# Performance work log

Measured on AMD Instinct MI355X. Metric: run time of the kernel, lower is better.

Reference implementation:

```python
import jax, jax.numpy as jnp
import numpy as np

T, S, F, A, POS = 32, 4096, 256, 64, 128


def setup_inputs() -> dict:
    key = jax.random.key(0)
    ks = jax.random.split(key, 12)
    sc = lambda fan_in: 1.0 / np.sqrt(fan_in)
    return {
        "batch_data": jax.random.normal(ks[0], (T * S, F), dtype=jnp.float32),
        "xywh": jax.random.uniform(ks[1], (T * S, 4), dtype=jnp.float32),
        # nn.Linear params (y = x @ W.T + b)
        "Wa": jax.random.uniform(ks[2], (A, F), minval=-sc(F), maxval=sc(F)),
        "ba": jax.random.uniform(ks[3], (A,), minval=-sc(F), maxval=sc(F)),
        "Wb": jax.random.uniform(ks[4], (A, F), minval=-sc(F), maxval=sc(F)),
        "bb": jax.random.uniform(ks[5], (A,), minval=-sc(F), maxval=sc(F)),
        "Wg": jax.random.uniform(ks[6], (F, F), minval=-sc(F), maxval=sc(F)),
        "bg": jax.random.uniform(ks[7], (F,), minval=-sc(F), maxval=sc(F)),
        "Wh": jax.random.uniform(ks[8], (POS, 2), minval=-sc(2), maxval=sc(2)),
        "bh": jax.random.uniform(ks[9], (POS,), minval=-sc(2), maxval=sc(2)),
    }


def reference(batch_data, xywh, Wa, ba, Wb, bb, Wg, bg, Wh, bh):
    x = batch_data.reshape(T, S, F)
    pos = xywh.reshape(T, S, -1)
    # positional embedding path (computed in original forward but unused in output)
    avg_pos = jnp.mean(pos, axis=0)            # [S, 4]
    rel_pos = pos[:, :, :2] - avg_pos[:, :2]   # [T, S, 2]
    _pos_embeds = rel_pos @ Wh.T + bh          # [T, S, POS] (dead, matches source)

    theta = x @ Wa.T + ba                      # [T, S, A]
    phi = x @ Wb.T + bb                        # [T, S, A]
    feats = x @ Wg.T + bg                      # [T, S, F]

    # per-object temporal attention: attn[s, t, u] = theta[t, s] . phi[u, s]
    attn = jnp.einsum('tsa,usa->stu', theta, phi)       # [S, T, T]
    out = jnp.einsum('stu,usf->tsf', attn, feats)       # [T, S, F]
    return out
```

## Files before the change

kernel.cpp:

```cpp
#include <hip/hip_runtime.h>

#define T_ 32
#define S_ 4096
#define F_ 256
#define A_ 64

typedef __attribute__((ext_vector_type(8))) short s8v;
typedef __attribute__((ext_vector_type(4))) float f4v;
typedef __attribute__((ext_vector_type(4))) short s4v;

#define MFMA(a, b, c) __builtin_amdgcn_mfma_f32_16x16x32_bf16((a), (b), (c), 0, 0, 0)

__device__ __forceinline__ unsigned short f2bf(float f) {
    unsigned int u = __builtin_bit_cast(unsigned int, f);
    u += 0x7FFFu + ((u >> 16) & 1u);
    return (unsigned short)(u >> 16);
}

__global__ void convert_weights(const float* __restrict__ Wa,
                                const float* __restrict__ Wb,
                                const float* __restrict__ Wg,
                                unsigned short* __restrict__ wsB)
{
    int base = (blockIdx.x * 256 + threadIdx.x) * 4;
    const float* src;
    if (base < 16384)      src = Wa + base;
    else if (base < 32768) src = Wb + (base - 16384);
    else                   src = Wg + (base - 32768);
    float4 v = *(const float4*)src;
    s4v p;
    p[0] = (short)f2bf(v.x); p[1] = (short)f2bf(v.y);
    p[2] = (short)f2bf(v.z); p[3] = (short)f2bf(v.w);
    *(s4v*)(wsB + base) = p;
}

#define XS_OFF 0
#define TH_OFF 16384
#define PH_OFF 20480
#define AT_OFF 24576
#define FT_OFF 26624
#define LDS_BYTES 43008

__global__ __launch_bounds__(256, 4) void fused_temporal(
    const float* __restrict__ X,
    const unsigned short* __restrict__ wsB,
    const float* __restrict__ ba, const float* __restrict__ bb,
    const float* __restrict__ bg,
    float* __restrict__ out)
{
    __shared__ alignas(16) unsigned char smem[LDS_BYTES];
    const int tid  = threadIdx.x;
    const int wave = tid >> 6;
    const int lane = tid & 63;
    const int quad = lane >> 4;
    const int l15  = lane & 15;
    const int s    = blockIdx.x;

    const unsigned short* WaB = wsB;
    const unsigned short* WbB = wsB + 16384;
    const unsigned short* WgB = wsB + 32768;

    float4 xv[8];
    #pragma unroll
    for (int i = 0; i < 4; ++i) {
        int linear = i * 256 + tid;
        int t = linear >> 5;
        int c = linear & 31;
        const float* xp = X + ((size_t)(t * S_ + s)) * F_ + c * 8;
        xv[2 * i]     = *(const float4*)(xp);
        xv[2 * i + 1] = *(const float4*)(xp + 4);
    }

    s8v wafrag[8], wbfrag[8];
    {
        const unsigned short* wa_row = WaB + (size_t)(16 * wave + l15) * F_ + quad * 8;
        const unsigned short* wb_row = WbB + (size_t)(16 * wave + l15) * F_ + quad * 8;
        #pragma unroll
        for (int ks = 0; ks < 8; ++ks) {
            wafrag[ks] = *(const s8v*)(wa_row + ks * 32);
            wbfrag[ks] = *(const s8v*)(wb_row + ks * 32);
        }
    }

    #pragma unroll
    for (int i = 0; i < 4; ++i) {
        int linear = i * 256 + tid;
        int t = linear >> 5;
        int c = linear & 31;
        float4 v0 = xv[2 * i];
        float4 v1 = xv[2 * i + 1];
        s8v p;
        p[0] = (short)f2bf(v0.x); p[1] = (short)f2bf(v0.y);
        p[2] = (short)f2bf(v0.z); p[3] = (short)f2bf(v0.w);
        p[4] = (short)f2bf(v1.x); p[5] = (short)f2bf(v1.y);
        p[6] = (short)f2bf(v1.z); p[7] = (short)f2bf(v1.w);
        *(s8v*)(&smem[XS_OFF + t * 512 + (((c + t) & 31) << 4)]) = p;
    }
    __syncthreads();

    s8v wg[2][8];
    {
        f4v ta0 = {0.f,0.f,0.f,0.f}, ta1 = {0.f,0.f,0.f,0.f};
        f4v pa0 = {0.f,0.f,0.f,0.f}, pa1 = {0.f,0.f,0.f,0.f};
        #pragma unroll
        for (int ks = 0; ks < 8; ++ks) {
            int chunk = 4 * ks + quad;
            s8v a0 = *(const s8v*)(&smem[XS_OFF + l15 * 512 + (((chunk + l15) & 31) << 4)]);
            s8v a1 = *(const s8v*)(&smem[XS_OFF + (l15 + 16) * 512 + (((chunk + l15 + 16) & 31) << 4)]);
            ta0 = MFMA(a0, wafrag[ks], ta0);
            ta1 = MFMA(a1, wafrag[ks], ta1);
            pa0 = MFMA(a0, wbfrag[ks], pa0);
            pa1 = MFMA(a1, wbfrag[ks], pa1);
        }

        #pragma unroll
        for (int g = 0; g < 2; ++g) {
            const unsigned short* wg_row = WgB + (size_t)(64 * wave + 16 * g + l15) * F_ + quad * 8;
            #pragma unroll
            for (int ks = 0; ks < 8; ++ks) wg[g][ks] = *(const s8v*)(wg_row + ks * 32);
        }

        float biasa = ba[16 * wave + l15];
        float biasb = bb[16 * wave + l15];
        int a_col = 16 * wave + l15;
        int chunk = a_col >> 3;
        int sub   = (a_col & 7) * 2;
        #pragma unroll
        for (int mt = 0; mt < 2; ++mt) {
            f4v va = mt ? ta1 : ta0;
            f4v vb = mt ? pa1 : pa0;
            #pragma unroll
            for (int r = 0; r < 4; ++r) {
                int t  = quad * 4 + r + 16 * mt;
                int sw = ((chunk + t) & 7) << 4;
                *(unsigned short*)(&smem[TH_OFF + t * 128 + sw + sub]) = f2bf(va[r] + biasa);
                *(unsigned short*)(&smem[PH_OFF + t * 128 + sw + sub]) = f2bf(vb[r] + biasb);
            }
        }
    }
    __syncthreads();

    {
        int mt2 = wave >> 1, nt2 = wave & 1;
        int t2 = l15 + 16 * mt2;
        int u2 = l15 + 16 * nt2;
        f4v acc2 = {0.f,0.f,0.f,0.f};
        #pragma unroll
        for (int ks = 0; ks < 2; ++ks) {
            int chunk = 4 * ks + quad;
            s8v av = *(const s8v*)(&smem[TH_OFF + t2 * 128 + (((chunk + t2) & 7) << 4)]);
            s8v bv = *(const s8v*)(&smem[PH_OFF + u2 * 128 + (((chunk + u2) & 7) << 4)]);
            acc2 = MFMA(av, bv, acc2);
        }
        int chunk = u2 >> 3;
        int sub   = (u2 & 7) * 2;
        #pragma unroll
        for (int r = 0; r < 4; ++r) {
            int tt = quad * 4 + r + 16 * mt2;
            *(unsigned short*)(&smem[AT_OFF + tt * 64 + (((chunk + tt) & 3) << 4) + sub]) = f2bf(acc2[r]);
        }
    }
    __syncthreads();

    {
        s8v battn[2];
        #pragma unroll
        for (int nt = 0; nt < 2; ++nt) {
            int t = l15 + 16 * nt;
            battn[nt] = *(const s8v*)(&smem[AT_OFF + t * 64 + (((quad + t) & 3) << 4)]);
        }

        #pragma unroll
        for (int g = 0; g < 4; ++g) {
            int n0 = 64 * wave + 16 * g;
            f4v fa0 = {0.f,0.f,0.f,0.f}, fa1 = {0.f,0.f,0.f,0.f};
            #pragma unroll
            for (int ks = 0; ks < 8; ++ks) {
                int chunk = 4 * ks + quad;
                s8v a0 = *(const s8v*)(&smem[XS_OFF + l15 * 512 + (((chunk + l15) & 31) << 4)]);
                s8v a1 = *(const s8v*)(&smem[XS_OFF + (l15 + 16) * 512 + (((chunk + l15 + 16) & 31) << 4)]);
                fa0 = MFMA(a0, wg[g & 1][ks], fa0);
                fa1 = MFMA(a1, wg[g & 1][ks], fa1);
            }
            if (g < 2) {
                const unsigned short* wg_row = WgB + (size_t)(64 * wave + 16 * (g + 2) + l15) * F_ + quad * 8;
                #pragma unroll
                for (int ks = 0; ks < 8; ++ks) wg[g & 1][ks] = *(const s8v*)(wg_row + ks * 32);
            }

            float biasg = bg[n0 + l15];
            int f = n0 + l15;
            #pragma unroll
            for (int mt = 0; mt < 2; ++mt) {
                f4v v = mt ? fa1 : fa0;
                int u0 = quad * 4 + 16 * mt;
                s4v pk;
                #pragma unroll
                for (int r = 0; r < 4; ++r) pk[r] = (short)f2bf(v[r] + biasg);
                int addr = FT_OFF + f * 64 + ((((u0 >> 3) + f) & 3) << 4) + (u0 & 7) * 2;
                *(s4v*)(&smem[addr]) = pk;
            }

            s8v av = *(const s8v*)(&smem[FT_OFF + f * 64 + (((quad + f) & 3) << 4)]);
            int f0 = n0 + 4 * quad;
            #pragma unroll
            for (int nt = 0; nt < 2; ++nt) {
                f4v z = {0.f,0.f,0.f,0.f};
                f4v acc = MFMA(av, battn[nt], z);
                int t = l15 + 16 * nt;
                float4 st;
                st.x = acc[0]; st.y = acc[1]; st.z = acc[2]; st.w = acc[3];
                *(float4*)(out + ((size_t)(t * S_ + s)) * F_ + f0) = st;
            }
        }
    }
}

extern "C" void kernel_launch(void* const* d_in, const int* in_sizes, int n_in,
                              void* d_out, int out_size, void* d_ws, size_t ws_size,
                              hipStream_t stream) {
    (void)in_sizes; (void)n_in; (void)ws_size; (void)out_size;
    const float* X  = (const float*)d_in[0];
    const float* Wa = (const float*)d_in[2];
    const float* ba = (const float*)d_in[3];
    const float* Wb = (const float*)d_in[4];
    const float* bb = (const float*)d_in[5];
    const float* Wg = (const float*)d_in[6];
    const float* bg = (const float*)d_in[7];
    float* out = (float*)d_out;
    unsigned short* wsB = (unsigned short*)d_ws;

    convert_weights<<<dim3(96), dim3(256), 0, stream>>>(Wa, Wb, Wg, wsB);
    fused_temporal<<<dim3(S_), dim3(256), 0, stream>>>(X, wsB, ba, bb, bg, out);
}
```

Before: 322.2 us.

## Process two objects per block to amortize weight fragment loads

Each block now handles two spatial positions (64 rows) instead of one, so every Wa/Wb/Wg fragment loaded from global memory feeds twice as many MFMAs. The LDS layout is reorganized so the feats staging area reuses the theta/phi region and is private to each wave. The grid is halved and launch bounds drop from 4 to 3 blocks per CU because of the larger LDS footprint and register use. The X prefetch is no longer overlapped with the weight loads, which may expose more memory latency.

```diff
diff --git a/kernel.cpp b/kernel.cpp
--- a/kernel.cpp
+++ b/kernel.cpp
@@ -4,6 +4,7 @@
 #define S_ 4096
 #define F_ 256
 #define A_ 64
+#define NS 2
 
 typedef __attribute__((ext_vector_type(8))) short s8v;
 typedef __attribute__((ext_vector_type(4))) float f4v;
@@ -35,13 +36,13 @@
 }
 
 #define XS_OFF 0
-#define TH_OFF 16384
-#define PH_OFF 20480
-#define AT_OFF 24576
-#define FT_OFF 26624
-#define LDS_BYTES 43008
-
-__global__ __launch_bounds__(256, 4) void fused_temporal(
+#define TH_OFF 32768
+#define PH_OFF 40960
+#define AT_OFF 49152
+#define FT_OFF 32768
+#define LDS_BYTES 53248
+
+__global__ __launch_bounds__(256, 3) void fused_temporal(
     const float* __restrict__ X,
     const unsigned short* __restrict__ wsB,
     const float* __restrict__ ba, const float* __restrict__ bb,
@@ -54,63 +55,59 @@
     const int lane = tid & 63;
     const int quad = lane >> 4;
     const int l15  = lane & 15;
-    const int s    = blockIdx.x;
+    const int s0   = blockIdx.x * NS;
 
     const unsigned short* WaB = wsB;
     const unsigned short* WbB = wsB + 16384;
     const unsigned short* WgB = wsB + 32768;
 
-    float4 xv[8];
     #pragma unroll
-    for (int i = 0; i < 4; ++i) {
+    for (int i = 0; i < 8; ++i) {
         int linear = i * 256 + tid;
-        int t = linear >> 5;
+        int r = linear >> 5;
         int c = linear & 31;
-        const float* xp = X + ((size_t)(t * S_ + s)) * F_ + c * 8;
-        xv[2 * i]     = *(const float4*)(xp);
-        xv[2 * i + 1] = *(const float4*)(xp + 4);
-    }
-
-    s8v wafrag[8], wbfrag[8];
-    {
-        const unsigned short* wa_row = WaB + (size_t)(16 * wave + l15) * F_ + quad * 8;
-        const unsigned short* wb_row = WbB + (size_t)(16 * wave + l15) * F_ + quad * 8;
-        #pragma unroll
-        for (int ks = 0; ks < 8; ++ks) {
-            wafrag[ks] = *(const s8v*)(wa_row + ks * 32);
-            wbfrag[ks] = *(const s8v*)(wb_row + ks * 32);
-        }
-    }
-
-    #pragma unroll
-    for (int i = 0; i < 4; ++i) {
-        int linear = i * 256 + tid;
-        int t = linear >> 5;
-        int c = linear & 31;
-        float4 v0 = xv[2 * i];
-        float4 v1 = xv[2 * i + 1];
+        int t  = r & 31;
+        int sl = r >> 5;
+        const float* xp = X + ((size_t)(t * S_ + s0 + sl)) * F_ + c * 8;
+        float4 v0 = *(const float4*)(xp);
+        float4 v1 = *(const float4*)(xp + 4);
         s8v p;
         p[0] = (short)f2bf(v0.x); p[1] = (short)f2bf(v0.y);
         p[2] = (short)f2bf(v0.z); p[3] = (short)f2bf(v0.w);
         p[4] = (short)f2bf(v1.x); p[5] = (short)f2bf(v1.y);
         p[6] = (short)f2bf(v1.z); p[7] = (short)f2bf(v1.w);
-        *(s8v*)(&smem[XS_OFF + t * 512 + (((c + t) & 31) << 4)]) = p;
+        *(s8v*)(&smem[XS_OFF + r * 512 + (((c + r) & 31) << 4)]) = p;
     }
     __syncthreads();
 
     s8v wg[2][8];
     {
-        f4v ta0 = {0.f,0.f,0.f,0.f}, ta1 = {0.f,0.f,0.f,0.f};
-        f4v pa0 = {0.f,0.f,0.f,0.f}, pa1 = {0.f,0.f,0.f,0.f};
+        const int n0 = 16 * wave;
+        s8v wafrag[8], wbfrag[8];
+        {
+            const unsigned short* wa_row = WaB + (size_t)(n0 + l15) * F_ + quad * 8;
+            const unsigned short* wb_row = WbB + (size_t)(n0 + l15) * F_ + quad * 8;
+            #pragma unroll
+            for (int ks = 0; ks < 8; ++ks) {
+                wafrag[ks] = *(const s8v*)(wa_row + ks * 32);
+                wbfrag[ks] = *(const s8v*)(wb_row + ks * 32);
+            }
+        }
+
+        f4v ta[4], pa[4];
+        #pragma unroll
+        for (int mt = 0; mt < 4; ++mt) { ta[mt] = f4v{0.f,0.f,0.f,0.f}; pa[mt] = f4v{0.f,0.f,0.f,0.f}; }
+
         #pragma unroll
         for (int ks = 0; ks < 8; ++ks) {
             int chunk = 4 * ks + quad;
-            s8v a0 = *(const s8v*)(&smem[XS_OFF + l15 * 512 + (((chunk + l15) & 31) << 4)]);
-            s8v a1 = *(const s8v*)(&smem[XS_OFF + (l15 + 16) * 512 + (((chunk + l15 + 16) & 31) << 4)]);
-            ta0 = MFMA(a0, wafrag[ks], ta0);
-            ta1 = MFMA(a1, wafrag[ks], ta1);
-            pa0 = MFMA(a0, wbfrag[ks], pa0);
-            pa1 = MFMA(a1, wbfrag[ks], pa1);
+            #pragma unroll
+            for (int mt = 0; mt < 4; ++mt) {
+                int r = 16 * mt + l15;
+                s8v a = *(const s8v*)(&smem[XS_OFF + r * 512 + (((chunk + r) & 31) << 4)]);
+                ta[mt] = MFMA(a, wafrag[ks], ta[mt]);
+                pa[mt] = MFMA(a, wbfrag[ks], pa[mt]);
+            }
         }
 
         #pragma unroll
@@ -120,67 +117,81 @@
             for (int ks = 0; ks < 8; ++ks) wg[g][ks] = *(const s8v*)(wg_row + ks * 32);
         }
 
-        float biasa = ba[16 * wave + l15];
-        float biasb = bb[16 * wave + l15];
-        int a_col = 16 * wave + l15;
+        float biasa = ba[n0 + l15];
+        float biasb = bb[n0 + l15];
+        int a_col = n0 + l15;
         int chunk = a_col >> 3;
         int sub   = (a_col & 7) * 2;
         #pragma unroll
-        for (int mt = 0; mt < 2; ++mt) {
-            f4v va = mt ? ta1 : ta0;
-            f4v vb = mt ? pa1 : pa0;
+        for (int mt = 0; mt < 4; ++mt) {
             #pragma unroll
             for (int r = 0; r < 4; ++r) {
-                int t  = quad * 4 + r + 16 * mt;
-                int sw = ((chunk + t) & 7) << 4;
-                *(unsigned short*)(&smem[TH_OFF + t * 128 + sw + sub]) = f2bf(va[r] + biasa);
-                *(unsigned short*)(&smem[PH_OFF + t * 128 + sw + sub]) = f2bf(vb[r] + biasb);
+                int row = 16 * mt + quad * 4 + r;
+                int sw  = ((chunk + row) & 7) << 4;
+                *(unsigned short*)(&smem[TH_OFF + row * 128 + sw + sub]) = f2bf(ta[mt][r] + biasa);
+                *(unsigned short*)(&smem[PH_OFF + row * 128 + sw + sub]) = f2bf(pa[mt][r] + biasb);
             }
         }
     }
     __syncthreads();
 
     {
-        int mt2 = wave >> 1, nt2 = wave & 1;
-        int t2 = l15 + 16 * mt2;
-        int u2 = l15 + 16 * nt2;
-        f4v acc2 = {0.f,0.f,0.f,0.f};
-        #pragma unroll
-        for (int ks = 0; ks < 2; ++ks) {
-            int chunk = 4 * ks + quad;
-            s8v av = *(const s8v*)(&smem[TH_OFF + t2 * 128 + (((chunk + t2) & 7) << 4)]);
-            s8v bv = *(const s8v*)(&smem[PH_OFF + u2 * 128 + (((chunk + u2) & 7) << 4)]);
-            acc2 = MFMA(av, bv, acc2);
-        }
-        int chunk = u2 >> 3;
-        int sub   = (u2 & 7) * 2;
-        #pragma unroll
-        for (int r = 0; r < 4; ++r) {
-            int tt = quad * 4 + r + 16 * mt2;
-            *(unsigned short*)(&smem[AT_OFF + tt * 64 + (((chunk + tt) & 3) << 4) + sub]) = f2bf(acc2[r]);
+        int sl  = wave >> 1;
+        int mt2 = wave & 1;
+        int t2  = l15 + 16 * mt2;
+        int rth = sl * 32 + t2;
+        #pragma unroll
+        for (int nt2 = 0; nt2 < 2; ++nt2) {
+            int u2  = l15 + 16 * nt2;
+            int rph = sl * 32 + u2;
+            f4v acc2 = {0.f,0.f,0.f,0.f};
+            #pragma unroll
+            for (int ks = 0; ks < 2; ++ks) {
+                int chunk = 4 * ks + quad;
+                s8v av = *(const s8v*)(&smem[TH_OFF + rth * 128 + (((chunk + rth) & 7) << 4)]);
+                s8v bv = *(const s8v*)(&smem[PH_OFF + rph * 128 + (((chunk + rph) & 7) << 4)]);
+                acc2 = MFMA(av, bv, acc2);
+            }
+            int chunk = u2 >> 3;
+            int sub   = (u2 & 7) * 2;
+            #pragma unroll
+            for (int r = 0; r < 4; ++r) {
+                int tt  = quad * 4 + r + 16 * mt2;
+                int rat = sl * 32 + tt;
+                *(unsigned short*)(&smem[AT_OFF + rat * 64 + (((chunk + rat) & 3) << 4) + sub]) = f2bf(acc2[r]);
+            }
         }
     }
     __syncthreads();
 
     {
-        s8v battn[2];
-        #pragma unroll
-        for (int nt = 0; nt < 2; ++nt) {
-            int t = l15 + 16 * nt;
-            battn[nt] = *(const s8v*)(&smem[AT_OFF + t * 64 + (((quad + t) & 3) << 4)]);
-        }
+        s8v battn[2][2];
+        #pragma unroll
+        for (int sl = 0; sl < 2; ++sl) {
+            #pragma unroll
+            for (int nt = 0; nt < 2; ++nt) {
+                int rat = sl * 32 + l15 + 16 * nt;
+                battn[sl][nt] = *(const s8v*)(&smem[AT_OFF + rat * 64 + (((quad + rat) & 3) << 4)]);
+            }
+        }
+
+        const int ftbase = FT_OFF + wave * 2048;
 
         #pragma unroll
         for (int g = 0; g < 4; ++g) {
             int n0 = 64 * wave + 16 * g;
-            f4v fa0 = {0.f,0.f,0.f,0.f}, fa1 = {0.f,0.f,0.f,0.f};
+            f4v fa[4];
+            #pragma unroll
+            for (int mt = 0; mt < 4; ++mt) fa[mt] = f4v{0.f,0.f,0.f,0.f};
             #pragma unroll
             for (int ks = 0; ks < 8; ++ks) {
                 int chunk = 4 * ks + quad;
-                s8v a0 = *(const s8v*)(&smem[XS_OFF + l15 * 512 + (((chunk + l15) & 31) << 4)]);
-                s8v a1 = *(const s8v*)(&smem[XS_OFF + (l15 + 16) * 512 + (((chunk + l15 + 16) & 31) << 4)]);
-                fa0 = MFMA(a0, wg[g & 1][ks], fa0);
-                fa1 = MFMA(a1, wg[g & 1][ks], fa1);
+                #pragma unroll
+                for (int mt = 0; mt < 4; ++mt) {
+                    int r = 16 * mt + l15;
+                    s8v a = *(const s8v*)(&smem[XS_OFF + r * 512 + (((chunk + r) & 31) << 4)]);
+                    fa[mt] = MFMA(a, wg[g & 1][ks], fa[mt]);
+                }
             }
             if (g < 2) {
                 const unsigned short* wg_row = WgB + (size_t)(64 * wave + 16 * (g + 2) + l15) * F_ + quad * 8;
@@ -189,28 +200,30 @@
             }
 
             float biasg = bg[n0 + l15];
-            int f = n0 + l15;
-            #pragma unroll
-            for (int mt = 0; mt < 2; ++mt) {
-                f4v v = mt ? fa1 : fa0;
-                int u0 = quad * 4 + 16 * mt;
+            #pragma unroll
+            for (int mt = 0; mt < 4; ++mt) {
+                int sl = mt >> 1;
+                int u0 = (mt & 1) * 16 + quad * 4;
                 s4v pk;
                 #pragma unroll
-                for (int r = 0; r < 4; ++r) pk[r] = (short)f2bf(v[r] + biasg);
-                int addr = FT_OFF + f * 64 + ((((u0 >> 3) + f) & 3) << 4) + (u0 & 7) * 2;
+                for (int r = 0; r < 4; ++r) pk[r] = (short)f2bf(fa[mt][r] + biasg);
+                int addr = ftbase + sl * 1024 + l15 * 64 + ((((u0 >> 3) + l15) & 3) << 4) + (u0 & 7) * 2;
                 *(s4v*)(&smem[addr]) = pk;
             }
 
-            s8v av = *(const s8v*)(&smem[FT_OFF + f * 64 + (((quad + f) & 3) << 4)]);
             int f0 = n0 + 4 * quad;
             #pragma unroll
-            for (int nt = 0; nt < 2; ++nt) {
-                f4v z = {0.f,0.f,0.f,0.f};
-                f4v acc = MFMA(av, battn[nt], z);
-                int t = l15 + 16 * nt;
-                float4 st;
-                st.x = acc[0]; st.y = acc[1]; st.z = acc[2]; st.w = acc[3];
-                *(float4*)(out + ((size_t)(t * S_ + s)) * F_ + f0) = st;
+            for (int sl = 0; sl < 2; ++sl) {
+                s8v avf = *(const s8v*)(&smem[ftbase + sl * 1024 + l15 * 64 + (((quad + l15) & 3) << 4)]);
+                #pragma unroll
+                for (int nt = 0; nt < 2; ++nt) {
+                    f4v z = {0.f,0.f,0.f,0.f};
+                    f4v acc = MFMA(avf, battn[sl][nt], z);
+                    int t = l15 + 16 * nt;
+                    float4 st;
+                    st.x = acc[0]; st.y = acc[1]; st.z = acc[2]; st.w = acc[3];
+                    *(float4*)(out + ((size_t)(t * S_ + s0 + sl)) * F_ + f0) = st;
+                }
             }
         }
     }
@@ -231,5 +244,5 @@
     unsigned short* wsB = (unsigned short*)d_ws;
 
     convert_weights<<<dim3(96), dim3(256), 0, stream>>>(Wa, Wb, Wg, wsB);
-    fused_temporal<<<dim3(S_), dim3(256), 0, stream>>>(X, wsB, ba, bb, bg, out);
-}
+    fused_temporal<<<dim3(S_ / NS), dim3(256), 0, stream>>>(X, wsB, ba, bb, bg, out);
+}
```

Result: faster. 314.6 us (-2.4%).
